# Performance work log

Hardware: AMD Instinct MI355X
Metric: run time of the kernel (lower is better)

Reference implementation:

```python
import jax, jax.numpy as jnp
import numpy as np

BS, NPTS, NM, D = 8, 8192, 32, 512  # objects, points/object, masks/object, feature dim


def setup_inputs() -> dict:
    key = jax.random.key(0)
    k1, k2, k3 = jax.random.split(key, 3)
    net_out = jax.random.normal(k1, (BS * NPTS, D), dtype=jnp.float32)
    mask_embs = jax.random.normal(k2, (BS * NM, D), dtype=jnp.float32)
    mask_pts = (jax.random.uniform(k3, (BS, NM, NPTS)) < 0.5).astype(jnp.float32)
    pt_offset = (jnp.arange(1, BS + 1) * NPTS).astype(jnp.int32)  # per-object end idx
    logit_scale = jnp.float32(2.6593)  # ln(1/0.07), CLIP-style
    return {
        "net_out": net_out,
        "mask_embs": mask_embs,
        "mask_pts": mask_pts,
        "logit_scale": logit_scale,
        "pt_offset": pt_offset,
    }


def reference(net_out, mask_embs, mask_pts, logit_scale, pt_offset):
    bs, nm, npts = mask_pts.shape
    d = net_out.shape[1]
    n_total = bs * nm

    # ragged per-object mask_pt @ net_out[start:end] -> uniform batched matmul
    net = net_out.reshape(bs, npts, d)
    sum_feats = jnp.einsum('bmp,bpd->bmd', mask_pts, net).reshape(n_total, d)

    mask_npts = jnp.sum(mask_pts, axis=-1).reshape(n_total, 1)  # points per mask
    nopts = (mask_npts[:, 0] == 0)                              # empty masks -> ignored
    avg_feats = sum_feats / (mask_npts + 1e-12)

    logits = (mask_embs @ avg_feats.T) * jnp.exp(logit_scale)   # [N, N]

    idx = jnp.arange(n_total)
    valid = ~nopts  # target == -100 (ignore) for empty masks, else arange diagonal
    texts_loss = jnp.where(valid, -jax.nn.log_softmax(logits, axis=-1)[idx, idx], 0.0)
    pts_loss = jnp.where(valid, -jax.nn.log_softmax(logits.T, axis=-1)[idx, idx], 0.0)

    def nonzero_avg(l):
        cnt = jnp.sum(l > 0)
        return jnp.where(cnt > 0, jnp.sum(l) / jnp.maximum(cnt, 1), 0.0)

    return (nonzero_avg(texts_loss) + nonzero_avg(pts_loss)) / 2.0
```

## Files before the change

### kernel.cpp

```cpp
#include <hip/hip_runtime.h>
#include <hip/hip_bf16.h>
#include <math.h>

#define BS 8
#define NPTS 8192
#define NM 32
#define D 512
#define NT (BS*NM)
#define KC 32
#define KCHUNK (NPTS/KC)
#define TILES (KCHUNK/32)
#define DC 8
#define DCHUNK (D/DC)
#define NWORDS (NPTS/32)

#define LOG2E 1.44269504088896f
#define LN2   0.69314718055995f

typedef short short8 __attribute__((ext_vector_type(8)));
typedef float f32x4 __attribute__((ext_vector_type(4)));

static constexpr size_t OFF_SUMF = 0;
static constexpr size_t OFF_CNTS = OFF_SUMF + (size_t)NT*D;
static constexpr size_t OFF_BITS = OFF_CNTS + NT;
static constexpr size_t OFF_LOG  = OFF_BITS + (size_t)NT*NWORDS;
static constexpr size_t OFF_RLSE = OFF_LOG + (size_t)NT*NT;
static constexpr size_t OFF_CLSE = OFF_RLSE + NT;

__device__ __forceinline__ short bf16_rne(float f) {
  return __builtin_bit_cast(short, __float2bfloat16(f));
}

#define GLOAD_LDS16(g, l) __builtin_amdgcn_global_load_lds( \
    (const __attribute__((address_space(1))) void*)(g),     \
    (__attribute__((address_space(3))) void*)(l), 16, 0, 0)

__global__ __launch_bounds__(256) void kp_prep(const float* __restrict__ mpts,
                                               unsigned int* __restrict__ mbits,
                                               float* __restrict__ cnts,
                                               float* __restrict__ sumf) {
  const int n = blockIdx.x;
  const int t = threadIdx.x;

  const float4* mp = (const float4*)(mpts + ((size_t)n << 13) + t * 32);
  unsigned int u = 0;
  #pragma unroll
  for (int q = 0; q < 8; ++q) {
    const float4 v = mp[q];
    u |= (v.x != 0.f ? 1u : 0u) << (q * 4 + 0);
    u |= (v.y != 0.f ? 1u : 0u) << (q * 4 + 1);
    u |= (v.z != 0.f ? 1u : 0u) << (q * 4 + 2);
    u |= (v.w != 0.f ? 1u : 0u) << (q * 4 + 3);
  }
  mbits[n * NWORDS + t] = u;

  ((float2*)(sumf + ((size_t)n << 9)))[t] = make_float2(0.f, 0.f);

  int c = __popc(u);
  #pragma unroll
  for (int o = 32; o > 0; o >>= 1) c += __shfl_down(c, o, 64);
  __shared__ int red[4];
  if ((t & 63) == 0) red[t >> 6] = c;
  __syncthreads();
  if (t == 0) cnts[n] = (float)(red[0] + red[1] + red[2] + red[3]);
}

__global__ __launch_bounds__(256, 8) void k1_mfma(const float* __restrict__ net,
                                                  const unsigned int* __restrict__ mbits,
                                                  float* __restrict__ sumf) {
  __shared__ float tile[2][32 * DCHUNK];
  const int bx = blockIdx.x;
  const int dc = bx & 7;
  const int kc = (bx >> 3) & 31;
  const int b  = bx >> 8;
  const int w    = threadIdx.x >> 6;
  const int lane = threadIdx.x & 63;
  const int lhi = lane >> 4, llo = lane & 15;
  const int k0 = kc * KCHUNK;

  auto stage = [&](int buf, int t) {
    const int kt = k0 + t * 32;
    #pragma unroll
    for (int si = 0; si < 2; ++si) {
      const int s = w * 2 + si;
      const int gsrc = (lane & 15) ^ (((s >> 1) & 3) << 2);
      const float* src = net
        + (((size_t)(b * NPTS + kt + s * 4 + (lane >> 4))) << 9)
        + dc * DCHUNK + (gsrc << 2);
      GLOAD_LDS16(src, &tile[buf][s * 256]);
    }
  };

  const unsigned int* r0 = mbits + (size_t)(b * NM + llo) * NWORDS + kc * TILES;
  const unsigned int* r1 = r0 + (size_t)16 * NWORDS;

  f32x4 acc0 = {0.f, 0.f, 0.f, 0.f};
  f32x4 acc1 = {0.f, 0.f, 0.f, 0.f};

  const int rbase = (lhi * 8) * 64 + ((((w * 4) + (llo >> 2)) ^ (lhi << 2)) << 2) + (llo & 3);
  const int sh = lhi * 8;

  stage(0, 0);
  __syncthreads();

  #pragma unroll
  for (int t = 0; t < TILES; ++t) {
    const int cur = t & 1;
    const unsigned int u0 = r0[t];
    const unsigned int u1 = r1[t];
    if (t + 1 < TILES) stage(cur ^ 1, t + 1);

    float bv[8];
    #pragma unroll
    for (int j = 0; j < 8; ++j) bv[j] = tile[cur][rbase + j * 64];

    short8 bf, a0f, a1f;
    #pragma unroll
    for (int j = 0; j < 8; ++j) bf[j] = bf16_rne(bv[j]);
    const unsigned int b0 = (u0 >> sh) & 0xffu;
    const unsigned int b1 = (u1 >> sh) & 0xffu;
    #pragma unroll
    for (int j = 0; j < 8; ++j) {
      a0f[j] = (short)(-(int)((b0 >> j) & 1u) & 0x3F80);
      a1f[j] = (short)(-(int)((b1 >> j) & 1u) & 0x3F80);
    }

    acc0 = __builtin_amdgcn_mfma_f32_16x16x32_bf16(a0f, bf, acc0, 0, 0, 0);
    acc1 = __builtin_amdgcn_mfma_f32_16x16x32_bf16(a1f, bf, acc1, 0, 0, 0);

    __syncthreads();
  }

  const int d0 = dc * DCHUNK + w * 16;
  float* sp = sumf + (((size_t)(b * NM)) << 9) + d0 + llo;
  #pragma unroll
  for (int j = 0; j < 4; ++j) {
    atomicAdd(sp + ((size_t)(lhi * 4 + j) << 9),      acc0[j]);
    atomicAdd(sp + ((size_t)(16 + lhi * 4 + j) << 9), acc1[j]);
  }
}

__global__ __launch_bounds__(64) void k2_logits(const float* __restrict__ embs,
                                                const float* __restrict__ sumf,
                                                const float* __restrict__ cnts,
                                                const float* __restrict__ lsc,
                                                float* __restrict__ logits) {
  const int lane = threadIdx.x;
  const int wt = blockIdx.x;
  const int ti = wt >> 4, tj = wt & 15;
  const int lhi = lane >> 4, llo = lane & 15;
  const float scale = expf(lsc[0]);

  const float* ea = embs + (((size_t)(ti * 16 + llo)) << 9) + lhi * 8;
  const float* sv = sumf + (((size_t)(tj * 16 + llo)) << 9) + lhi * 8;
  f32x4 acc = {0.f, 0.f, 0.f, 0.f};
  #pragma unroll 4
  for (int kk = 0; kk < D / 32; ++kk) {
    const float4 e0 = *(const float4*)(ea);
    const float4 e1 = *(const float4*)(ea + 4);
    const float4 v0 = *(const float4*)(sv);
    const float4 v1 = *(const float4*)(sv + 4);
    const float ev[8] = {e0.x, e0.y, e0.z, e0.w, e1.x, e1.y, e1.z, e1.w};
    const float vv[8] = {v0.x, v0.y, v0.z, v0.w, v1.x, v1.y, v1.z, v1.w};
    short8 ef, vf;
    #pragma unroll
    for (int j = 0; j < 8; ++j) { ef[j] = bf16_rne(ev[j]); vf[j] = bf16_rne(vv[j]); }
    acc = __builtin_amdgcn_mfma_f32_16x16x32_bf16(ef, vf, acc, 0, 0, 0);
    ea += 32; sv += 32;
  }
  const float invc = scale / (cnts[tj * 16 + llo] + 1e-12f);
  float* lp = logits + (size_t)(ti * 16) * NT + tj * 16 + llo;
  #pragma unroll
  for (int r = 0; r < 4; ++r)
    lp[(size_t)(lhi * 4 + r) * NT] = acc[r] * invc;
}

__global__ __launch_bounds__(256) void k3_lse(const float* __restrict__ logits,
                                              float* __restrict__ rowlse,
                                              float* __restrict__ clse) {
  const int g = blockIdx.x;
  const int r = threadIdx.x >> 4;
  const int c = threadIdx.x & 15;
  __shared__ float red[16][17];
  if (g < 16) {
    const int col = g * 16 + c;
    float mx = -1e30f;
    #pragma unroll 4
    for (int kk = 0; kk < 16; ++kk)
      mx = fmaxf(mx, logits[(size_t)(kk * 16 + r) * NT + col]);
    red[r][c] = mx; __syncthreads();
    for (int st = 8; st; st >>= 1) { if (r < st) red[r][c] = fmaxf(red[r][c], red[r + st][c]); __syncthreads(); }
    const float mx2 = red[0][c] * LOG2E; __syncthreads();
    float s = 0.f;
    #pragma unroll 4
    for (int kk = 0; kk < 16; ++kk)
      s += exp2f(logits[(size_t)(kk * 16 + r) * NT + col] * LOG2E - mx2);
    red[r][c] = s; __syncthreads();
    for (int st = 8; st; st >>= 1) { if (r < st) red[r][c] += red[r + st][c]; __syncthreads(); }
    if (r == 0) clse[col] = (mx2 + log2f(red[0][c])) * LN2;
  } else {
    const int row = (g - 16) * 16 + r;
    float mx = -1e30f;
    #pragma unroll 4
    for (int kk = 0; kk < 16; ++kk)
      mx = fmaxf(mx, logits[(size_t)row * NT + kk * 16 + c]);
    #pragma unroll
    for (int o = 8; o; o >>= 1) mx = fmaxf(mx, __shfl_xor(mx, o, 64));
    const float mx2 = mx * LOG2E;
    float s = 0.f;
    #pragma unroll 4
    for (int kk = 0; kk < 16; ++kk)
      s += exp2f(logits[(size_t)row * NT + kk * 16 + c] * LOG2E - mx2);
    #pragma unroll
    for (int o = 8; o; o >>= 1) s += __shfl_xor(s, o, 64);
    if (c == 0) rowlse[row] = (mx2 + log2f(s)) * LN2;
  }
}

__global__ __launch_bounds__(256) void k4_loss(const float* __restrict__ logits,
                                               const float* __restrict__ rowlse,
                                               const float* __restrict__ clse,
                                               const float* __restrict__ cnts,
                                               float* __restrict__ out) {
  const int i = threadIdx.x;
  const float diag = logits[(size_t)i * NT + i];
  const bool valid = cnts[i] > 0.f;
  const float tl = valid ? (rowlse[i] - diag) : 0.f;
  const float pl = valid ? (clse[i] - diag) : 0.f;

  __shared__ float red[4][256];
  red[0][i] = tl;
  red[1][i] = (tl > 0.f) ? 1.f : 0.f;
  red[2][i] = pl;
  red[3][i] = (pl > 0.f) ? 1.f : 0.f;
  __syncthreads();
  for (int st = 128; st > 0; st >>= 1) {
    if (i < st) {
      red[0][i] += red[0][i + st];
      red[1][i] += red[1][i + st];
      red[2][i] += red[2][i + st];
      red[3][i] += red[3][i + st];
    }
    __syncthreads();
  }
  if (i == 0) {
    const float a1 = (red[1][0] > 0.f) ? red[0][0] / fmaxf(red[1][0], 1.f) : 0.f;
    const float a2 = (red[3][0] > 0.f) ? red[2][0] / fmaxf(red[3][0], 1.f) : 0.f;
    out[0] = 0.5f * (a1 + a2);
  }
}

extern "C" void kernel_launch(void* const* d_in, const int* in_sizes, int n_in,
                              void* d_out, int out_size, void* d_ws, size_t ws_size,
                              hipStream_t stream) {
  const float* net  = (const float*)d_in[0];
  const float* embs = (const float*)d_in[1];
  const float* mpts = (const float*)d_in[2];
  const float* lsc  = (const float*)d_in[3];

  float* ws     = (float*)d_ws;
  float* sumf   = ws + OFF_SUMF;
  float* cnts   = ws + OFF_CNTS;
  unsigned int* mbits = (unsigned int*)(ws + OFF_BITS);
  float* logits = ws + OFF_LOG;
  float* rowlse = ws + OFF_RLSE;
  float* clse   = ws + OFF_CLSE;
  float* outp   = (float*)d_out;

  kp_prep<<<dim3(NT), dim3(256), 0, stream>>>(mpts, mbits, cnts, sumf);
  k1_mfma<<<dim3(BS * KC * DC), dim3(256), 0, stream>>>(net, mbits, sumf);
  k2_logits<<<dim3(NT), dim3(64), 0, stream>>>(embs, sumf, cnts, lsc, logits);
  k3_lse<<<dim3(32), dim3(256), 0, stream>>>(logits, rowlse, clse);
  k4_loss<<<dim3(1), dim3(256), 0, stream>>>(logits, rowlse, clse, cnts, outp);
}
```

Before: 52.54 us.

## Restructure segment matmul per-wave staging and fuse LSE into logits and loss kernels

The segment-sum kernel now works on half as many K chunks per block. Each wave stages its own slice of net_out through a double buffer into LDS and paces it with explicit waitcnt instead of block-wide barriers. The mask words are preloaded as vectors, and bit pairs are swapped to match a new XOR-swizzled LDS read pattern. The logits kernel now computes a 16x256 row block per workgroup and fuses the row log-sum-exp into it. The column log-sum-exp moves into the single-block loss kernel, so one launch goes away but that block does a serial 256-element column scan per thread.

Measured after the change: 108.9 us. 2.07x slower.

```diff
diff --git a/kernel.cpp b/kernel.cpp
--- a/kernel.cpp
+++ b/kernel.cpp
@@ -6,12 +6,11 @@
 #define NPTS 8192
 #define NM 32
 #define D 512
-#define NT (BS*NM)
-#define KC 32
+#define NT 256
+#define KC 16
 #define KCHUNK (NPTS/KC)
 #define TILES (KCHUNK/32)
 #define DC 8
-#define DCHUNK (D/DC)
 #define NWORDS (NPTS/32)
 
 #define LOG2E 1.44269504088896f
@@ -25,7 +24,6 @@
 static constexpr size_t OFF_BITS = OFF_CNTS + NT;
 static constexpr size_t OFF_LOG  = OFF_BITS + (size_t)NT*NWORDS;
 static constexpr size_t OFF_RLSE = OFF_LOG + (size_t)NT*NT;
-static constexpr size_t OFF_CLSE = OFF_RLSE + NT;
 
 __device__ __forceinline__ short bf16_rne(float f) {
   return __builtin_bit_cast(short, __float2bfloat16(f));
@@ -41,7 +39,6 @@
                                                float* __restrict__ sumf) {
   const int n = blockIdx.x;
   const int t = threadIdx.x;
-
   const float4* mp = (const float4*)(mpts + ((size_t)n << 13) + t * 32);
   unsigned int u = 0;
   #pragma unroll
@@ -53,9 +50,7 @@
     u |= (v.w != 0.f ? 1u : 0u) << (q * 4 + 3);
   }
   mbits[n * NWORDS + t] = u;
-
   ((float2*)(sumf + ((size_t)n << 9)))[t] = make_float2(0.f, 0.f);
-
   int c = __popc(u);
   #pragma unroll
   for (int o = 32; o > 0; o >>= 1) c += __shfl_down(c, o, 64);
@@ -65,74 +60,91 @@
   if (t == 0) cnts[n] = (float)(red[0] + red[1] + red[2] + red[3]);
 }
 
-__global__ __launch_bounds__(256, 8) void k1_mfma(const float* __restrict__ net,
+__global__ __launch_bounds__(256, 4) void k1_mfma(const float* __restrict__ net,
                                                   const unsigned int* __restrict__ mbits,
                                                   float* __restrict__ sumf) {
-  __shared__ float tile[2][32 * DCHUNK];
+  __shared__ float wt[4][2][512];
   const int bx = blockIdx.x;
   const int dc = bx & 7;
-  const int kc = (bx >> 3) & 31;
-  const int b  = bx >> 8;
+  const int kc = (bx >> 3) & 15;
+  const int b  = bx >> 7;
   const int w    = threadIdx.x >> 6;
   const int lane = threadIdx.x & 63;
   const int lhi = lane >> 4, llo = lane & 15;
+  const int par = lhi & 1;
   const int k0 = kc * KCHUNK;
-
-  auto stage = [&](int buf, int t) {
-    const int kt = k0 + t * 32;
-    #pragma unroll
-    for (int si = 0; si < 2; ++si) {
-      const int s = w * 2 + si;
-      const int gsrc = (lane & 15) ^ (((s >> 1) & 3) << 2);
-      const float* src = net
-        + (((size_t)(b * NPTS + kt + s * 4 + (lane >> 4))) << 9)
-        + dc * DCHUNK + (gsrc << 2);
-      GLOAD_LDS16(src, &tile[buf][s * 256]);
-    }
-  };
-
-  const unsigned int* r0 = mbits + (size_t)(b * NM + llo) * NWORDS + kc * TILES;
-  const unsigned int* r1 = r0 + (size_t)16 * NWORDS;
+  const int d0w = dc * 64 + w * 16;
+
+  const unsigned int* r0p = mbits + (size_t)(b * NM + llo) * NWORDS + kc * TILES;
+  const uint4 m00 = *(const uint4*)(r0p + 0);
+  const uint4 m01 = *(const uint4*)(r0p + 4);
+  const uint4 m02 = *(const uint4*)(r0p + 8);
+  const uint4 m03 = *(const uint4*)(r0p + 12);
+  const unsigned int* r1p = r0p + (size_t)16 * NWORDS;
+  const uint4 m10 = *(const uint4*)(r1p + 0);
+  const uint4 m11 = *(const uint4*)(r1p + 4);
+  const uint4 m12 = *(const uint4*)(r1p + 8);
+  const uint4 m13 = *(const uint4*)(r1p + 12);
+  const unsigned int w0[16] = {m00.x,m00.y,m00.z,m00.w, m01.x,m01.y,m01.z,m01.w,
+                               m02.x,m02.y,m02.z,m02.w, m03.x,m03.y,m03.z,m03.w};
+  const unsigned int w1[16] = {m10.x,m10.y,m10.z,m10.w, m11.x,m11.y,m11.z,m11.w,
+                               m12.x,m12.y,m12.z,m12.w, m13.x,m13.y,m13.z,m13.w};
+
+  const float* s0 = net + ((size_t)(b * NPTS + k0 + (lane >> 2)) << 9)
+                        + d0w + ((lane & 3) << 2);
+  const float* s1 = s0 + ((size_t)16 << 9);
 
   f32x4 acc0 = {0.f, 0.f, 0.f, 0.f};
   f32x4 acc1 = {0.f, 0.f, 0.f, 0.f};
 
-  const int rbase = (lhi * 8) * 64 + ((((w * 4) + (llo >> 2)) ^ (lhi << 2)) << 2) + (llo & 3);
-  const int sh = lhi * 8;
-
-  stage(0, 0);
-  __syncthreads();
+  GLOAD_LDS16(s0, &wt[w][0][0]);
+  GLOAD_LDS16(s1, &wt[w][0][256]);
+  s0 += (size_t)32 << 9; s1 += (size_t)32 << 9;
+
+  const int rb = lhi * 128 + (par << 4) + llo;
+  const float* wtw = &wt[w][0][0];
 
   #pragma unroll
   for (int t = 0; t < TILES; ++t) {
     const int cur = t & 1;
-    const unsigned int u0 = r0[t];
-    const unsigned int u1 = r1[t];
-    if (t + 1 < TILES) stage(cur ^ 1, t + 1);
-
-    float bv[8];
-    #pragma unroll
-    for (int j = 0; j < 8; ++j) bv[j] = tile[cur][rbase + j * 64];
+    if (t > 0) {
+      asm volatile("s_waitcnt lgkmcnt(0)" ::: "memory");
+    }
+    if (t + 1 < TILES) {
+      GLOAD_LDS16(s0, &wt[w][cur ^ 1][0]);
+      GLOAD_LDS16(s1, &wt[w][cur ^ 1][256]);
+      s0 += (size_t)32 << 9; s1 += (size_t)32 << 9;
+      asm volatile("s_waitcnt vmcnt(2)" ::: "memory");
+    } else {
+      asm volatile("s_waitcnt vmcnt(0)" ::: "memory");
+    }
+    __builtin_amdgcn_sched_barrier(0);
+
+    float bp[8];
+    #pragma unroll
+    for (int j = 0; j < 8; ++j) bp[j] = wtw[(size_t)cur * 512 + (rb ^ (j << 4))];
 
     short8 bf, a0f, a1f;
     #pragma unroll
-    for (int j = 0; j < 8; ++j) bf[j] = bf16_rne(bv[j]);
-    const unsigned int b0 = (u0 >> sh) & 0xffu;
-    const unsigned int b1 = (u1 >> sh) & 0xffu;
+    for (int j = 0; j < 8; ++j) bf[j] = bf16_rne(bp[j]);
+
+    unsigned int us0 = (w0[t] >> (lhi * 8)) & 0xffu;
+    unsigned int us1 = (w1[t] >> (lhi * 8)) & 0xffu;
+    const unsigned int sw0 = ((us0 & 0x55u) << 1) | ((us0 >> 1) & 0x55u);
+    const unsigned int sw1 = ((us1 & 0x55u) << 1) | ((us1 >> 1) & 0x55u);
+    us0 = par ? sw0 : us0;
+    us1 = par ? sw1 : us1;
     #pragma unroll
     for (int j = 0; j < 8; ++j) {
-      a0f[j] = (short)(-(int)((b0 >> j) & 1u) & 0x3F80);
-      a1f[j] = (short)(-(int)((b1 >> j) & 1u) & 0x3F80);
+      a0f[j] = (short)(-(int)((us0 >> j) & 1u) & 0x3F80);
+      a1f[j] = (short)(-(int)((us1 >> j) & 1u) & 0x3F80);
     }
 
     acc0 = __builtin_amdgcn_mfma_f32_16x16x32_bf16(a0f, bf, acc0, 0, 0, 0);
     acc1 = __builtin_amdgcn_mfma_f32_16x16x32_bf16(a1f, bf, acc1, 0, 0, 0);
-
-    __syncthreads();
-  }
-
-  const int d0 = dc * DCHUNK + w * 16;
-  float* sp = sumf + (((size_t)(b * NM)) << 9) + d0 + llo;
+  }
+
+  float* sp = sumf + (((size_t)(b * NM)) << 9) + d0w + llo;
   #pragma unroll
   for (int j = 0; j < 4; ++j) {
     atomicAdd(sp + ((size_t)(lhi * 4 + j) << 9),      acc0[j]);
@@ -140,93 +152,114 @@
   }
 }
 
-__global__ __launch_bounds__(64) void k2_logits(const float* __restrict__ embs,
-                                                const float* __restrict__ sumf,
-                                                const float* __restrict__ cnts,
-                                                const float* __restrict__ lsc,
-                                                float* __restrict__ logits) {
-  const int lane = threadIdx.x;
-  const int wt = blockIdx.x;
-  const int ti = wt >> 4, tj = wt & 15;
+__global__ __launch_bounds__(256) void k2_logits(const float* __restrict__ embs,
+                                                 const float* __restrict__ sumf,
+                                                 const float* __restrict__ cnts,
+                                                 const float* __restrict__ lsc,
+                                                 float* __restrict__ logits,
+                                                 float* __restrict__ rowlse) {
+  const int i0 = blockIdx.x * 16;
+  const int w = threadIdx.x >> 6, lane = threadIdx.x & 63;
   const int lhi = lane >> 4, llo = lane & 15;
-  const float scale = expf(lsc[0]);
-
-  const float* ea = embs + (((size_t)(ti * 16 + llo)) << 9) + lhi * 8;
-  const float* sv = sumf + (((size_t)(tj * 16 + llo)) << 9) + lhi * 8;
-  f32x4 acc = {0.f, 0.f, 0.f, 0.f};
+
+  const float* ea = embs + ((size_t)(i0 + llo) << 9) + lhi * 8;
+  const float* sv = sumf + ((size_t)(w * 64 + llo) << 9) + lhi * 8;
+  f32x4 acc[4] = {{0.f,0.f,0.f,0.f},{0.f,0.f,0.f,0.f},{0.f,0.f,0.f,0.f},{0.f,0.f,0.f,0.f}};
   #pragma unroll 4
-  for (int kk = 0; kk < D / 32; ++kk) {
+  for (int kk = 0; kk < 16; ++kk) {
     const float4 e0 = *(const float4*)(ea);
     const float4 e1 = *(const float4*)(ea + 4);
-    const float4 v0 = *(const float4*)(sv);
-    const float4 v1 = *(const float4*)(sv + 4);
-    const float ev[8] = {e0.x, e0.y, e0.z, e0.w, e1.x, e1.y, e1.z, e1.w};
-    const float vv[8] = {v0.x, v0.y, v0.z, v0.w, v1.x, v1.y, v1.z, v1.w};
-    short8 ef, vf;
-    #pragma unroll
-    for (int j = 0; j < 8; ++j) { ef[j] = bf16_rne(ev[j]); vf[j] = bf16_rne(vv[j]); }
-    acc = __builtin_amdgcn_mfma_f32_16x16x32_bf16(ef, vf, acc, 0, 0, 0);
+    const float ev[8] = {e0.x,e0.y,e0.z,e0.w,e1.x,e1.y,e1.z,e1.w};
+    short8 af;
+    #pragma unroll
+    for (int j = 0; j < 8; ++j) af[j] = bf16_rne(ev[j]);
+    #pragma unroll
+    for (int tj = 0; tj < 4; ++tj) {
+      const float* p = sv + ((size_t)tj << 13);
+      const float4 v0 = *(const float4*)(p);
+      const float4 v1 = *(const float4*)(p + 4);
+      const float vv[8] = {v0.x,v0.y,v0.z,v0.w,v1.x,v1.y,v1.z,v1.w};
+      short8 vf;
+      #pragma unroll
+      for (int j = 0; j < 8; ++j) vf[j] = bf16_rne(vv[j]);
+      acc[tj] = __builtin_amdgcn_mfma_f32_16x16x32_bf16(af, vf, acc[tj], 0, 0, 0);
+    }
     ea += 32; sv += 32;
   }
-  const float invc = scale / (cnts[tj * 16 + llo] + 1e-12f);
-  float* lp = logits + (size_t)(ti * 16) * NT + tj * 16 + llo;
-  #pragma unroll
-  for (int r = 0; r < 4; ++r)
-    lp[(size_t)(lhi * 4 + r) * NT] = acc[r] * invc;
-}
-
-__global__ __launch_bounds__(256) void k3_lse(const float* __restrict__ logits,
-                                              float* __restrict__ rowlse,
-                                              float* __restrict__ clse) {
-  const int g = blockIdx.x;
-  const int r = threadIdx.x >> 4;
-  const int c = threadIdx.x & 15;
-  __shared__ float red[16][17];
-  if (g < 16) {
-    const int col = g * 16 + c;
-    float mx = -1e30f;
-    #pragma unroll 4
-    for (int kk = 0; kk < 16; ++kk)
-      mx = fmaxf(mx, logits[(size_t)(kk * 16 + r) * NT + col]);
-    red[r][c] = mx; __syncthreads();
-    for (int st = 8; st; st >>= 1) { if (r < st) red[r][c] = fmaxf(red[r][c], red[r + st][c]); __syncthreads(); }
-    const float mx2 = red[0][c] * LOG2E; __syncthreads();
-    float s = 0.f;
-    #pragma unroll 4
-    for (int kk = 0; kk < 16; ++kk)
-      s += exp2f(logits[(size_t)(kk * 16 + r) * NT + col] * LOG2E - mx2);
-    red[r][c] = s; __syncthreads();
-    for (int st = 8; st; st >>= 1) { if (r < st) red[r][c] += red[r + st][c]; __syncthreads(); }
-    if (r == 0) clse[col] = (mx2 + log2f(red[0][c])) * LN2;
-  } else {
-    const int row = (g - 16) * 16 + r;
-    float mx = -1e30f;
-    #pragma unroll 4
-    for (int kk = 0; kk < 16; ++kk)
-      mx = fmaxf(mx, logits[(size_t)row * NT + kk * 16 + c]);
-    #pragma unroll
-    for (int o = 8; o; o >>= 1) mx = fmaxf(mx, __shfl_xor(mx, o, 64));
-    const float mx2 = mx * LOG2E;
-    float s = 0.f;
-    #pragma unroll 4
-    for (int kk = 0; kk < 16; ++kk)
-      s += exp2f(logits[(size_t)row * NT + kk * 16 + c] * LOG2E - mx2);
-    #pragma unroll
-    for (int o = 8; o; o >>= 1) s += __shfl_xor(s, o, 64);
-    if (c == 0) rowlse[row] = (mx2 + log2f(s)) * LN2;
-  }
-}
-
-__global__ __launch_bounds__(256) void k4_loss(const float* __restrict__ logits,
+
+  const float scale = expf(lsc[0]);
+  float lg[4][4];
+  #pragma unroll
+  for (int tj = 0; tj < 4; ++tj) {
+    const int c = w * 64 + tj * 16 + llo;
+    const float ic = scale / (cnts[c] + 1e-12f);
+    #pragma unroll
+    for (int r = 0; r < 4; ++r) lg[tj][r] = acc[tj][r] * ic;
+  }
+  float* lp = logits + (size_t)i0 * NT;
+  #pragma unroll
+  for (int tj = 0; tj < 4; ++tj)
+    #pragma unroll
+    for (int r = 0; r < 4; ++r)
+      lp[(size_t)(lhi * 4 + r) * NT + w * 64 + tj * 16 + llo] = lg[tj][r];
+
+  __shared__ float sred[2][4][16];
+  __shared__ float gmax[16];
+  float pm[4];
+  #pragma unroll
+  for (int r = 0; r < 4; ++r) {
+    pm[r] = fmaxf(fmaxf(lg[0][r], lg[1][r]), fmaxf(lg[2][r], lg[3][r]));
+    #pragma unroll
+    for (int o = 1; o < 16; o <<= 1) pm[r] = fmaxf(pm[r], __shfl_xor(pm[r], o, 64));
+  }
+  if (llo == 0) {
+    #pragma unroll
+    for (int r = 0; r < 4; ++r) sred[0][w][lhi * 4 + r] = pm[r];
+  }
+  __syncthreads();
+  if (threadIdx.x < 16)
+    gmax[threadIdx.x] = fmaxf(fmaxf(sred[0][0][threadIdx.x], sred[0][1][threadIdx.x]),
+                              fmaxf(sred[0][2][threadIdx.x], sred[0][3][threadIdx.x]));
+  __syncthreads();
+  float ps[4];
+  #pragma unroll
+  for (int r = 0; r < 4; ++r) {
+    const float m2 = gmax[lhi * 4 + r] * LOG2E;
+    ps[r] = exp2f(lg[0][r] * LOG2E - m2) + exp2f(lg[1][r] * LOG2E - m2)
+          + exp2f(lg[2][r] * LOG2E - m2) + exp2f(lg[3][r] * LOG2E - m2);
+    #pragma unroll
+    for (int o = 1; o < 16; o <<= 1) ps[r] += __shfl_xor(ps[r], o, 64);
+  }
+  if (llo == 0) {
+    #pragma unroll
+    for (int r = 0; r < 4; ++r) sred[1][w][lhi * 4 + r] = ps[r];
+  }
+  __syncthreads();
+  if (threadIdx.x < 16) {
+    const float s = sred[1][0][threadIdx.x] + sred[1][1][threadIdx.x]
+                  + sred[1][2][threadIdx.x] + sred[1][3][threadIdx.x];
+    rowlse[i0 + threadIdx.x] = (gmax[threadIdx.x] * LOG2E + log2f(s)) * LN2;
+  }
+}
+
+__global__ __launch_bounds__(256) void k3_loss(const float* __restrict__ logits,
                                                const float* __restrict__ rowlse,
-                                               const float* __restrict__ clse,
                                                const float* __restrict__ cnts,
                                                float* __restrict__ out) {
   const int i = threadIdx.x;
+  float mc = -1e30f;
+  #pragma unroll 8
+  for (int k = 0; k < NT; ++k) mc = fmaxf(mc, logits[(size_t)k * NT + i]);
+  const float m2 = mc * LOG2E;
+  float sc = 0.f;
+  #pragma unroll 8
+  for (int k = 0; k < NT; ++k) sc += exp2f(logits[(size_t)k * NT + i] * LOG2E - m2);
+  const float collse = (m2 + log2f(sc)) * LN2;
+
   const float diag = logits[(size_t)i * NT + i];
   const bool valid = cnts[i] > 0.f;
   const float tl = valid ? (rowlse[i] - diag) : 0.f;
-  const float pl = valid ? (clse[i] - diag) : 0.f;
+  const float pl = valid ? (collse - diag) : 0.f;
 
   __shared__ float red[4][256];
   red[0][i] = tl;
@@ -264,12 +297,10 @@
   unsigned int* mbits = (unsigned int*)(ws + OFF_BITS);
   float* logits = ws + OFF_LOG;
   float* rowlse = ws + OFF_RLSE;
-  float* clse   = ws + OFF_CLSE;
   float* outp   = (float*)d_out;
 
   kp_prep<<<dim3(NT), dim3(256), 0, stream>>>(mpts, mbits, cnts, sumf);
   k1_mfma<<<dim3(BS * KC * DC), dim3(256), 0, stream>>>(net, mbits, sumf);
-  k2_logits<<<dim3(NT), dim3(64), 0, stream>>>(embs, sumf, cnts, lsc, logits);
-  k3_lse<<<dim3(32), dim3(256), 0, stream>>>(logits, rowlse, clse);
-  k4_loss<<<dim3(1), dim3(256), 0, stream>>>(logits, rowlse, clse, cnts, outp);
-}
+  k2_logits<<<dim3(16), dim3(256), 0, stream>>>(embs, sumf, cnts, lsc, logits, rowlse);
+  k3_loss<<<dim3(1), dim3(256), 0, stream>>>(logits, rowlse, cnts, outp);
+}
```
